# Kernel optimization log

Hardware: AMD Instinct MI355X
Metric: run time of the kernel (lower is better)

## Reference

```python
import jax, jax.numpy as jnp
import numpy as np

M = 16                      # multiplicity of each irrep block
INV3 = 1.0 / np.sqrt(3.0)   # w3j(1,1,0) component-normalized
INV2 = 1.0 / np.sqrt(2.0)   # w3j(1,1,1) component-normalized
A0 = 1.0 / np.sqrt(2.0 * M) # fan-in norm for 0e outputs (2 paths x mul 16)
A1 = 1.0 / np.sqrt(3.0 * M) # fan-in norm for 1o outputs (3 paths x mul 16)


def setup_inputs() -> dict:
    E, N, ED, HID = 100000, 10000, 32, 128
    WNUM = 2 * M * (2 * M) + 3 * M * M  # 1792 per-edge TP weights
    ks = jax.random.split(jax.random.key(0), 10)
    return {
        "dst": jax.random.randint(ks[0], (E,), 0, N),
        "x_src": jax.random.normal(ks[1], (E, 4 * M), jnp.float32),   # 16x0e+16x1o
        "x_dst": jax.random.normal(ks[2], (N, 4 * M), jnp.float32),
        "sh": jax.random.normal(ks[3], (E, 4), jnp.float32),          # 1x0e+1x1o
        "edge_attr": jax.random.normal(ks[4], (E, ED), jnp.float32),
        "We1": jax.random.normal(ks[5], (ED, HID), jnp.float32) / np.sqrt(ED),
        "be1": jnp.zeros((HID,), jnp.float32),
        "We2": jax.random.normal(ks[6], (HID, WNUM), jnp.float32) / np.sqrt(HID),
        "be2": jnp.zeros((WNUM,), jnp.float32),
        "Wr0": jax.random.normal(ks[7], (M, 2 * M), jnp.float32),     # 16x0e -> 32x0e
        "Wr1": jax.random.normal(ks[8], (M, M), jnp.float32),         # 16x1o -> 16x1o
    }


def _forward(dst, x_src, x_dst, sh, edge_attr, We1, be1, We2, be2, Wr0, Wr1):
    E = x_src.shape[0]
    N = x_dst.shape[0]
    o0 = 2 * M  # 32x0e tp output (scalars + gates)

    # edge MLP -> per-edge tensor-product weights [E, 1792]
    w = jax.nn.relu(edge_attr @ We1 + be1) @ We2 + be2
    i = 0
    w_ss = w[:, i:i + M * o0].reshape(E, M, o0); i += M * o0   # 0e x 0e -> 0e
    w_vv0 = w[:, i:i + M * o0].reshape(E, M, o0); i += M * o0  # 1o x 1o -> 0e
    w_sv = w[:, i:i + M * M].reshape(E, M, M); i += M * M      # 0e x 1o -> 1o
    w_vs = w[:, i:i + M * M].reshape(E, M, M); i += M * M      # 1o x 0e -> 1o
    w_vv1 = w[:, i:i + M * M].reshape(E, M, M)                 # 1o x 1o -> 1o

    s1 = x_src[:, :M]                       # [E, 16]
    v1 = x_src[:, M:].reshape(E, M, 3)      # [E, 16, 3]
    s2 = sh[:, 0]                           # [E]
    v2 = sh[:, 1:4]                         # [E, 3]

    # fully-connected tensor product with per-edge weights
    out0 = A0 * (jnp.einsum('em,emo->eo', s1 * s2[:, None], w_ss)
                 + INV3 * jnp.einsum('emc,ec,emo->eo', v1, v2, w_vv0))  # [E, 32]
    cross = jnp.cross(v1, v2[:, None, :])   # [E, 16, 3]
    out1 = A1 * (jnp.einsum('em,ec,emo->eoc', s1, v2, w_sv)
                 + jnp.einsum('emc,e,emo->eoc', v1, s2, w_vs)
                 + INV2 * jnp.einsum('emc,emo->eoc', cross, w_vv1))     # [E, 16, 3]
    msg = jnp.concatenate([out0, out1.reshape(E, -1)], axis=1)          # [E, 80]

    # scatter-mean over destination nodes
    ssum = jax.ops.segment_sum(msg, dst, num_segments=N)
    cnt = jax.ops.segment_sum(jnp.ones((E,), msg.dtype), dst, num_segments=N)
    msg = ssum / jnp.maximum(cnt, 1.0)[:, None]                          # [N, 80]

    # residual equivariant linear on x_dst
    sd = x_dst[:, :M]
    vd = x_dst[:, M:].reshape(N, M, 3)
    res0 = (sd @ Wr0) / np.sqrt(M)                                       # [N, 32]
    res1 = jnp.einsum('nmc,mo->noc', vd, Wr1) / np.sqrt(M)               # [N, 16, 3]
    msg = msg + jnp.concatenate([res0, res1.reshape(N, -1)], axis=1)

    # gate nonlinearity: relu(scalars), sigmoid(gates) * gated vectors
    scalars = jax.nn.relu(msg[:, :M])
    gates = jax.nn.sigmoid(msg[:, M:2 * M])
    gated = msg[:, 2 * M:].reshape(N, M, 3) * gates[:, :, None]
    return jnp.concatenate([scalars, gated.reshape(N, -1)], axis=1)      # [N, 64]


def reference(dst, x_src, x_dst, sh, edge_attr, We1, be1, We2, be2, Wr0, Wr1):
    return _forward(dst, x_src, x_dst, sh, edge_attr, We1, be1, We2, be2, Wr0, Wr1)
```

## Files before the change

### kernel.cpp

```cpp
#include <hip/hip_runtime.h>
#include <math.h>

#define WNUM 1792
#define HID 128

#define INV3C 0.5773502691896258f
#define INV2C 0.7071067811865476f
#define A0C   0.17677669529663687f
#define A1C   0.14433756729740643f
#define MAXDEG 64

typedef short bf8 __attribute__((ext_vector_type(8)));
typedef _Float16 f16x8 __attribute__((ext_vector_type(8)));
typedef _Float16 f16x4 __attribute__((ext_vector_type(4)));
typedef float f32x4 __attribute__((ext_vector_type(4)));

__device__ inline unsigned short f2bf(float f) {
  union { float f; unsigned u; } v; v.f = f;
  unsigned r = v.u + 0x7FFFu + ((v.u >> 16) & 1u);
  return (unsigned short)(r >> 16);
}
__device__ inline float bf2f(unsigned short h) {
  union { unsigned u; float f; } v; v.u = ((unsigned)h) << 16;
  return v.f;
}
__device__ inline float wscale(int t) {
  if (t < 32) return A0C;
  if (t < 64) return A0C * INV3C;
  if (t < 96) return A1C;
  return A1C * INV2C;
}

__global__ __launch_bounds__(256) void prep_kernel(
    const float* __restrict__ We1, const float* __restrict__ We2,
    const float* __restrict__ be2,
    unsigned short* __restrict__ we1x, _Float16* __restrict__ we2h,
    float* __restrict__ be2p, int* __restrict__ cntp, int N)
{
  int i = blockIdx.x * 256 + threadIdx.x;
  if (i < 28672) {
    int t = i >> 8, c = (i >> 6) & 3, lane = i & 63;
    int quad = lane >> 4, l15 = lane & 15;
    int col = t * 16 + l15;
    float sc = wscale(t);
    f16x8 v;
    #pragma unroll
    for (int j = 0; j < 8; ++j) {
      int k = c * 32 + quad * 8 + j;
      v[j] = (_Float16)(We2[(size_t)k * WNUM + col] * sc);
    }
    *(f16x8*)(we2h + (size_t)t * 2048 + c * 512 + lane * 8) = v;
  } else if (i < 29184) {
    int q = i - 28672;
    int c1 = q >> 6, lane = q & 63;
    int quad = lane >> 4, l15 = lane & 15;
    int col = c1 * 16 + l15;
    bf8 hh, ll;
    #pragma unroll
    for (int j = 0; j < 8; ++j) {
      int k = quad * 8 + j;
      float v = We1[k * HID + col];
      unsigned short hi = f2bf(v);
      hh[j] = (short)hi;
      ll[j] = (short)f2bf(v - bf2f(hi));
    }
    *(bf8*)(we1x + c1 * 1024 + lane * 8) = hh;
    *(bf8*)(we1x + c1 * 1024 + 512 + lane * 8) = ll;
  } else if (i < 30976) {
    int q = i - 29184;
    int t = q >> 4, l16 = q & 15;
    be2p[(t >> 1) * 32 + l16 * 2 + (t & 1)] = be2[q] * wscale(t);
  } else if (i < 30976 + N) {
    cntp[i - 30976] = 0;
  }
}

__device__ inline void chains2(const f16x8* a0, const f16x8* a1,
    f16x8 b0, f16x8 b1, f16x8 b2, f16x8 b3,
    f16x8 b4, f16x8 b5, f16x8 b6, f16x8 b7,
    float2 bias, f32x4* wa, f32x4* wb)
{
  f32x4 ca0 = {bias.x, bias.x, bias.x, bias.x};
  f32x4 cb0 = {bias.y, bias.y, bias.y, bias.y};
  f32x4 ca1 = ca0, cb1 = cb0;
  ca0 = __builtin_amdgcn_mfma_f32_16x16x32_f16(a0[0], b0, ca0, 0, 0, 0);
  cb0 = __builtin_amdgcn_mfma_f32_16x16x32_f16(a0[0], b4, cb0, 0, 0, 0);
  ca1 = __builtin_amdgcn_mfma_f32_16x16x32_f16(a1[0], b0, ca1, 0, 0, 0);
  cb1 = __builtin_amdgcn_mfma_f32_16x16x32_f16(a1[0], b4, cb1, 0, 0, 0);
  ca0 = __builtin_amdgcn_mfma_f32_16x16x32_f16(a0[1], b1, ca0, 0, 0, 0);
  cb0 = __builtin_amdgcn_mfma_f32_16x16x32_f16(a0[1], b5, cb0, 0, 0, 0);
  ca1 = __builtin_amdgcn_mfma_f32_16x16x32_f16(a1[1], b1, ca1, 0, 0, 0);
  cb1 = __builtin_amdgcn_mfma_f32_16x16x32_f16(a1[1], b5, cb1, 0, 0, 0);
  ca0 = __builtin_amdgcn_mfma_f32_16x16x32_f16(a0[2], b2, ca0, 0, 0, 0);
  cb0 = __builtin_amdgcn_mfma_f32_16x16x32_f16(a0[2], b6, cb0, 0, 0, 0);
  ca1 = __builtin_amdgcn_mfma_f32_16x16x32_f16(a1[2], b2, ca1, 0, 0, 0);
  cb1 = __builtin_amdgcn_mfma_f32_16x16x32_f16(a1[2], b6, cb1, 0, 0, 0);
  ca0 = __builtin_amdgcn_mfma_f32_16x16x32_f16(a0[3], b3, ca0, 0, 0, 0);
  cb0 = __builtin_amdgcn_mfma_f32_16x16x32_f16(a0[3], b7, cb0, 0, 0, 0);
  ca1 = __builtin_amdgcn_mfma_f32_16x16x32_f16(a1[3], b3, ca1, 0, 0, 0);
  cb1 = __builtin_amdgcn_mfma_f32_16x16x32_f16(a1[3], b7, cb1, 0, 0, 0);
  wa[0] = ca0; wb[0] = cb0; wa[1] = ca1; wb[1] = cb1;
}

#define LOADB_LDS(BASE) \
  f16x8 b0 = *(const f16x8*)((BASE)); \
  f16x8 b1 = *(const f16x8*)((BASE) + 512); \
  f16x8 b2 = *(const f16x8*)((BASE) + 1024); \
  f16x8 b3 = *(const f16x8*)((BASE) + 1536); \
  f16x8 b4 = *(const f16x8*)((BASE) + 2048); \
  f16x8 b5 = *(const f16x8*)((BASE) + 2560); \
  f16x8 b6 = *(const f16x8*)((BASE) + 3072); \
  f16x8 b7 = *(const f16x8*)((BASE) + 3584);

template <bool MSG>
__global__ __launch_bounds__(256, 2) void edge_kernel(
    const float* __restrict__ ea, const float* __restrict__ xsrc,
    const float* __restrict__ sh, const int* __restrict__ dst,
    const float* __restrict__ be1,
    const unsigned short* __restrict__ we1x, const _Float16* __restrict__ we2h,
    const float* __restrict__ be2p,
    float* __restrict__ outp,
    int* __restrict__ eidx, int* __restrict__ cntp, int E)
{
  const int lane = threadIdx.x & 63;
  const int w    = threadIdx.x >> 6;
  const int quad = lane >> 4;
  const int l16  = lane & 15;
  const int eb   = (blockIdx.x * 4 + w) * 32;

  __shared__ _Float16 Bsm[2][4096];
  __shared__ _Float16 h_s[4][32][136];
  __shared__ _Float16 fss_s[4][16][32];
  __shared__ _Float16 fvv_s[4][16][32];
  __shared__ _Float16 s1h_s[4][16][32];
  __shared__ _Float16 v1h_s[4][16][3][32];
  __shared__ float4 vq_s[4][32];

  #define STAGEB(ldsbuf, p) { \
    const _Float16* gsrc_ = we2h + (size_t)(p) * 4096; \
    __builtin_amdgcn_global_load_lds( \
      (const __attribute__((address_space(1))) void*)(gsrc_ + (w * 2) * 512 + lane * 8), \
      (__attribute__((address_space(3))) void*)((ldsbuf) + (w * 2) * 512), 16, 0, 0); \
    __builtin_amdgcn_global_load_lds( \
      (const __attribute__((address_space(1))) void*)(gsrc_ + (w * 2 + 1) * 512 + lane * 8), \
      (__attribute__((address_space(3))) void*)((ldsbuf) + (w * 2 + 1) * 512), 16, 0, 0); \
  }

  if (lane < 32) {
    int ge = eb + lane;
    if (ge < E) {
      int node = dst[ge];
      int pos = atomicAdd(cntp + node, 1);
      if (MSG) { if (pos < MAXDEG) eidx[node * MAXDEG + pos] = ge; }
    }
  }

  {
    int e2 = lane >> 1, mg = lane & 1;
    int ge = eb + e2;
    if (ge < E) {
      const float* xp = xsrc + (size_t)ge * 64;
      float4 sq0 = *(const float4*)(xp + mg * 8);
      float4 sq1 = *(const float4*)(xp + mg * 8 + 4);
      float s1a[8] = {sq0.x,sq0.y,sq0.z,sq0.w,sq1.x,sq1.y,sq1.z,sq1.w};
      const float* vp = xp + 16 + mg * 24;
      float la[24];
      #pragma unroll
      for (int qv = 0; qv < 6; ++qv) {
        float4 t = *(const float4*)(vp + qv * 4);
        la[qv*4+0] = t.x; la[qv*4+1] = t.y; la[qv*4+2] = t.z; la[qv*4+3] = t.w;
      }
      float4 shq = *(const float4*)(sh + (size_t)ge * 4);
      float s2 = shq.x, v2x = shq.y, v2y = shq.z, v2z = shq.w;
      #pragma unroll
      for (int mi = 0; mi < 8; ++mi) {
        int m = mg * 8 + mi;
        float v1x = la[mi*3], v1y = la[mi*3+1], v1z = la[mi*3+2];
        fss_s[w][m][e2] = (_Float16)(s1a[mi] * s2);
        fvv_s[w][m][e2] = (_Float16)(v1x*v2x + v1y*v2y + v1z*v2z);
        s1h_s[w][m][e2] = (_Float16)s1a[mi];
        v1h_s[w][m][0][e2] = (_Float16)v1x;
        v1h_s[w][m][1][e2] = (_Float16)v1y;
        v1h_s[w][m][2][e2] = (_Float16)v1z;
      }
      if (mg == 0) vq_s[w][e2] = make_float4(v2x, v2y, v2z, s2);
    } else {
      #pragma unroll
      for (int mi = 0; mi < 8; ++mi) {
        int m = mg * 8 + mi;
        fss_s[w][m][e2] = (_Float16)0.f;
        fvv_s[w][m][e2] = (_Float16)0.f;
        s1h_s[w][m][e2] = (_Float16)0.f;
        v1h_s[w][m][0][e2] = (_Float16)0.f;
        v1h_s[w][m][1][e2] = (_Float16)0.f;
        v1h_s[w][m][2][e2] = (_Float16)0.f;
      }
      if (mg == 0) vq_s[w][e2] = make_float4(0,0,0,0);
    }
  }

  {
    bf8 ah[2], al[2];
    #pragma unroll
    for (int g = 0; g < 2; ++g) {
      int gea = eb + g * 16 + l16; if (gea > E - 1) gea = E - 1;
      const float* ep = ea + (size_t)gea * 32 + quad * 8;
      float4 p0 = *(const float4*)ep;
      float4 p1 = *(const float4*)(ep + 4);
      float pv[8] = {p0.x,p0.y,p0.z,p0.w,p1.x,p1.y,p1.z,p1.w};
      #pragma unroll
      for (int j = 0; j < 8; ++j) {
        unsigned short hi = f2bf(pv[j]);
        ah[g][j] = (short)hi;
        al[g][j] = (short)f2bf(pv[j] - bf2f(hi));
      }
    }
    const unsigned short* wb1 = we1x + lane * 8;
    #pragma unroll 2
    for (int c = 0; c < 8; ++c) {
      bf8 bh = *(const bf8*)(wb1 + c * 1024);
      bf8 bl = *(const bf8*)(wb1 + c * 1024 + 512);
      float bias = be1[c * 16 + l16];
      #pragma unroll
      for (int g = 0; g < 2; ++g) {
        f32x4 hc = {bias, bias, bias, bias};
        hc = __builtin_amdgcn_mfma_f32_16x16x32_bf16(al[g], bh, hc, 0, 0, 0);
        hc = __builtin_amdgcn_mfma_f32_16x16x32_bf16(ah[g], bl, hc, 0, 0, 0);
        hc = __builtin_amdgcn_mfma_f32_16x16x32_bf16(ah[g], bh, hc, 0, 0, 0);
        #pragma unroll
        for (int r = 0; r < 4; ++r)
          h_s[w][g * 16 + quad * 4 + r][c * 16 + l16] = (_Float16)fmaxf(hc[r], 0.f);
      }
    }
  }

  STAGEB(&Bsm[0][0], 0)
  __syncthreads();

  f16x8 af[2][4];
  #pragma unroll
  for (int g = 0; g < 2; ++g)
    #pragma unroll
    for (int ch = 0; ch < 4; ++ch)
      af[g][ch] = *(const f16x8*)&h_s[w][g * 16 + l16][ch * 32 + quad * 8];

  const float* bp = be2p + l16 * 2;

  float m0a[2][4] = {{0,0,0,0},{0,0,0,0}}, m0b[2][4] = {{0,0,0,0},{0,0,0,0}};
  int p = 0;

  #pragma unroll 1
  for (int i = 0; i < 16; ++i) {
    STAGEB(&Bsm[(p + 1) & 1][0], p + 1)
    const _Float16* bL = &Bsm[p & 1][lane * 8];
    LOADB_LDS(bL)
    float2 bias2 = *(const float2*)(bp + p * 32);
    f32x4 wa[2], wb[2];
    chains2(af[0], af[1], b0,b1,b2,b3,b4,b5,b6,b7, bias2, wa, wb);
    #pragma unroll
    for (int g = 0; g < 2; ++g) {
      f16x4 fv = *(const f16x4*)&fss_s[w][i][g * 16 + quad * 4];
      #pragma unroll
      for (int r = 0; r < 4; ++r) {
        float f = (float)fv[r];
        m0a[g][r] = fmaf(wa[g][r], f, m0a[g][r]);
        m0b[g][r] = fmaf(wb[g][r], f, m0b[g][r]);
      }
    }
    __syncthreads();
    ++p;
  }

  #pragma unroll 1
  for (int i = 0; i < 16; ++i) {
    STAGEB(&Bsm[(p + 1) & 1][0], p + 1)
    const _Float16* bL = &Bsm[p & 1][lane * 8];
    LOADB_LDS(bL)
    float2 bias2 = *(const float2*)(bp + p * 32);
    f32x4 wa[2], wb[2];
    chains2(af[0], af[1], b0,b1,b2,b3,b4,b5,b6,b7, bias2, wa, wb);
    #pragma unroll
    for (int g = 0; g < 2; ++g) {
      f16x4 fv = *(const f16x4*)&fvv_s[w][i][g * 16 + quad * 4];
      #pragma unroll
      for (int r = 0; r < 4; ++r) {
        float f = (float)fv[r];
        m0a[g][r] = fmaf(wa[g][r], f, m0a[g][r]);
        m0b[g][r] = fmaf(wb[g][r], f, m0b[g][r]);
      }
    }
    __syncthreads();
    ++p;
  }

  #pragma unroll
  for (int g = 0; g < 2; ++g)
    #pragma unroll
    for (int r = 0; r < 4; ++r) {
      int ge = eb + g * 16 + quad * 4 + r;
      if (ge < E) {
        if (MSG) {
          float* mp = outp + (size_t)ge * 80;
          mp[l16]      = m0a[g][r];
          mp[16 + l16] = m0b[g][r];
        } else {
          float* ap = outp + (size_t)dst[ge] * 80;
          atomicAdd(ap + l16,      m0a[g][r]);
          atomicAdd(ap + 16 + l16, m0b[g][r]);
        }
      }
    }

  float sg[2][4] = {{0,0,0,0},{0,0,0,0}};
  #pragma unroll 1
  for (int i = 0; i < 8; ++i) {
    STAGEB(&Bsm[(p + 1) & 1][0], p + 1)
    const _Float16* bL = &Bsm[p & 1][lane * 8];
    LOADB_LDS(bL)
    float2 bias2 = *(const float2*)(bp + p * 32);
    f32x4 wa[2], wb[2];
    chains2(af[0], af[1], b0,b1,b2,b3,b4,b5,b6,b7, bias2, wa, wb);
    #pragma unroll
    for (int g = 0; g < 2; ++g) {
      f16x4 sA = *(const f16x4*)&s1h_s[w][2*i][g * 16 + quad * 4];
      f16x4 sB = *(const f16x4*)&s1h_s[w][2*i + 1][g * 16 + quad * 4];
      #pragma unroll
      for (int r = 0; r < 4; ++r)
        sg[g][r] = fmaf(wb[g][r], (float)sB[r], fmaf(wa[g][r], (float)sA[r], sg[g][r]));
    }
    __syncthreads();
    ++p;
  }
  float4 vq[2][4];
  #pragma unroll
  for (int g = 0; g < 2; ++g)
    #pragma unroll
    for (int r = 0; r < 4; ++r) vq[g][r] = vq_s[w][g * 16 + quad * 4 + r];

  float m1x[2][4], m1y[2][4], m1z[2][4];
  #pragma unroll
  for (int g = 0; g < 2; ++g)
    #pragma unroll
    for (int r = 0; r < 4; ++r) {
      m1x[g][r] = sg[g][r] * vq[g][r].x;
      m1y[g][r] = sg[g][r] * vq[g][r].y;
      m1z[g][r] = sg[g][r] * vq[g][r].z;
    }

  {
    float ux[2][4] = {{0,0,0,0},{0,0,0,0}}, uy[2][4] = {{0,0,0,0},{0,0,0,0}},
          uz[2][4] = {{0,0,0,0},{0,0,0,0}};
    #pragma unroll 1
    for (int i = 0; i < 8; ++i) {
      STAGEB(&Bsm[(p + 1) & 1][0], p + 1)
      const _Float16* bL = &Bsm[p & 1][lane * 8];
      LOADB_LDS(bL)
      float2 bias2 = *(const float2*)(bp + p * 32);
      f32x4 wa[2], wb[2];
      chains2(af[0], af[1], b0,b1,b2,b3,b4,b5,b6,b7, bias2, wa, wb);
      #pragma unroll
      for (int g = 0; g < 2; ++g) {
        f16x4 xA = *(const f16x4*)&v1h_s[w][2*i][0][g*16 + quad*4];
        f16x4 xB = *(const f16x4*)&v1h_s[w][2*i+1][0][g*16 + quad*4];
        f16x4 yA = *(const f16x4*)&v1h_s[w][2*i][1][g*16 + quad*4];
        f16x4 yB = *(const f16x4*)&v1h_s[w][2*i+1][1][g*16 + quad*4];
        f16x4 zA = *(const f16x4*)&v1h_s[w][2*i][2][g*16 + quad*4];
        f16x4 zB = *(const f16x4*)&v1h_s[w][2*i+1][2][g*16 + quad*4];
        #pragma unroll
        for (int r = 0; r < 4; ++r) {
          ux[g][r] = fmaf(wb[g][r], (float)xB[r], fmaf(wa[g][r], (float)xA[r], ux[g][r]));
          uy[g][r] = fmaf(wb[g][r], (float)yB[r], fmaf(wa[g][r], (float)yA[r], uy[g][r]));
          uz[g][r] = fmaf(wb[g][r], (float)zB[r], fmaf(wa[g][r], (float)zA[r], uz[g][r]));
        }
      }
      __syncthreads();
      ++p;
    }
    #pragma unroll
    for (int g = 0; g < 2; ++g)
      #pragma unroll
      for (int r = 0; r < 4; ++r) {
        m1x[g][r] = fmaf(vq[g][r].w, ux[g][r], m1x[g][r]);
        m1y[g][r] = fmaf(vq[g][r].w, uy[g][r], m1y[g][r]);
        m1z[g][r] = fmaf(vq[g][r].w, uz[g][r], m1z[g][r]);
      }
  }

  {
    float ux[2][4] = {{0,0,0,0},{0,0,0,0}}, uy[2][4] = {{0,0,0,0},{0,0,0,0}},
          uz[2][4] = {{0,0,0,0},{0,0,0,0}};
    #pragma unroll 1
    for (int i = 0; i < 8; ++i) {
      if (p + 1 < 56) STAGEB(&Bsm[(p + 1) & 1][0], p + 1)
      const _Float16* bL = &Bsm[p & 1][lane * 8];
      LOADB_LDS(bL)
      float2 bias2 = *(const float2*)(bp + p * 32);
      f32x4 wa[2], wb[2];
      chains2(af[0], af[1], b0,b1,b2,b3,b4,b5,b6,b7, bias2, wa, wb);
      #pragma unroll
      for (int g = 0; g < 2; ++g) {
        f16x4 xA = *(const f16x4*)&v1h_s[w][2*i][0][g*16 + quad*4];
        f16x4 xB = *(const f16x4*)&v1h_s[w][2*i+1][0][g*16 + quad*4];
        f16x4 yA = *(const f16x4*)&v1h_s[w][2*i][1][g*16 + quad*4];
        f16x4 yB = *(const f16x4*)&v1h_s[w][2*i+1][1][g*16 + quad*4];
        f16x4 zA = *(const f16x4*)&v1h_s[w][2*i][2][g*16 + quad*4];
        f16x4 zB = *(const f16x4*)&v1h_s[w][2*i+1][2][g*16 + quad*4];
        #pragma unroll
        for (int r = 0; r < 4; ++r) {
          ux[g][r] = fmaf(wb[g][r], (float)xB[r], fmaf(wa[g][r], (float)xA[r], ux[g][r]));
          uy[g][r] = fmaf(wb[g][r], (float)yB[r], fmaf(wa[g][r], (float)yA[r], uy[g][r]));
          uz[g][r] = fmaf(wb[g][r], (float)zB[r], fmaf(wa[g][r], (float)zA[r], uz[g][r]));
        }
      }
      __syncthreads();
      ++p;
    }
    #pragma unroll
    for (int g = 0; g < 2; ++g)
      #pragma unroll
      for (int r = 0; r < 4; ++r) {
        m1x[g][r] = fmaf(uy[g][r], vq[g][r].z, m1x[g][r]);
        m1x[g][r] = fmaf(-uz[g][r], vq[g][r].y, m1x[g][r]);
        m1y[g][r] = fmaf(uz[g][r], vq[g][r].x, m1y[g][r]);
        m1y[g][r] = fmaf(-ux[g][r], vq[g][r].z, m1y[g][r]);
        m1z[g][r] = fmaf(ux[g][r], vq[g][r].y, m1z[g][r]);
        m1z[g][r] = fmaf(-uy[g][r], vq[g][r].x, m1z[g][r]);
      }
  }

  #pragma unroll
  for (int g = 0; g < 2; ++g)
    #pragma unroll
    for (int r = 0; r < 4; ++r) {
      int ge = eb + g * 16 + quad * 4 + r;
      if (ge < E) {
        if (MSG) {
          float* mp = outp + (size_t)ge * 80;
          mp[32 + l16*3 + 0] = m1x[g][r];
          mp[32 + l16*3 + 1] = m1y[g][r];
          mp[32 + l16*3 + 2] = m1z[g][r];
        } else {
          float* ap = outp + (size_t)dst[ge] * 80;
          atomicAdd(ap + 32 + l16*3 + 0, m1x[g][r]);
          atomicAdd(ap + 32 + l16*3 + 1, m1y[g][r]);
          atomicAdd(ap + 32 + l16*3 + 2, m1z[g][r]);
        }
      }
    }
  #undef STAGEB
}

__global__ __launch_bounds__(128) void node_gather_kernel(
    const float* __restrict__ msg, const int* __restrict__ eidx,
    const int* __restrict__ cntp,
    const float* __restrict__ xdst, const float* __restrict__ Wr0,
    const float* __restrict__ Wr1, float* __restrict__ out, int N)
{
  int n = blockIdx.x;
  if (n >= N) return;
  int j = threadIdx.x;
  int c0 = cntp[n];
  int deg = c0 < MAXDEG ? c0 : MAXDEG;
  float inv = 1.0f / fmaxf((float)c0, 1.0f);
  __shared__ float s_sum[80];
  if (j < 80) {
    float s = 0.f;
    const int* ep = eidx + (size_t)n * MAXDEG;
    int i = 0;
    for (; i + 1 < deg; i += 2) {
      int e0 = ep[i], e1 = ep[i + 1];
      s += msg[(size_t)e0 * 80 + j] + msg[(size_t)e1 * 80 + j];
    }
    if (i < deg) s += msg[(size_t)ep[i] * 80 + j];
    s_sum[j] = s * inv;
  }
  __syncthreads();
  if (j >= 64) return;
  const float* xd = xdst + (size_t)n * 64;
  float* op = out + (size_t)n * 64;
  if (j < 16) {
    float s = 0.f;
    #pragma unroll
    for (int m = 0; m < 16; ++m) s = fmaf(xd[m], Wr0[m * 32 + j], s);
    op[j] = fmaxf(s_sum[j] + 0.25f * s, 0.f);
  } else {
    int jj = j - 16;
    int o = (jj * 86) >> 8;
    int c = jj - o * 3;
    float tg = 0.f, v = 0.f;
    #pragma unroll
    for (int m = 0; m < 16; ++m) {
      tg = fmaf(xd[m], Wr0[m * 32 + 16 + o], tg);
      v  = fmaf(xd[16 + m * 3 + c], Wr1[m * 16 + o], v);
    }
    float g = 1.0f / (1.0f + expf(-(s_sum[16 + o] + 0.25f * tg)));
    op[16 + jj] = (s_sum[32 + jj] + 0.25f * v) * g;
  }
}

__global__ __launch_bounds__(256) void node_kernel(
    const float* __restrict__ accn, const int* __restrict__ cntp,
    const float* __restrict__ xdst, const float* __restrict__ Wr0,
    const float* __restrict__ Wr1, float* __restrict__ out, int N)
{
  int idx = blockIdx.x * 256 + threadIdx.x;
  int n = idx >> 6, j = idx & 63;
  if (n >= N) return;
  float inv = 1.0f / fmaxf((float)cntp[n], 1.0f);
  const float* ap = accn + (size_t)n * 80;
  const float* xd = xdst + (size_t)n * 64;
  float* op = out + (size_t)n * 64;
  if (j < 16) {
    float s = 0.f;
    #pragma unroll
    for (int m = 0; m < 16; ++m) s = fmaf(xd[m], Wr0[m * 32 + j], s);
    op[j] = fmaxf(ap[j] * inv + 0.25f * s, 0.f);
  } else {
    int jj = j - 16;
    int o = (jj * 86) >> 8;
    int c = jj - o * 3;
    float tg = 0.f, v = 0.f;
    #pragma unroll
    for (int m = 0; m < 16; ++m) {
      tg = fmaf(xd[m], Wr0[m * 32 + 16 + o], tg);
      v  = fmaf(xd[16 + m * 3 + c], Wr1[m * 16 + o], v);
    }
    float g = 1.0f / (1.0f + expf(-(ap[16 + o] * inv + 0.25f * tg)));
    op[16 + jj] = (ap[32 + jj] * inv + 0.25f * v) * g;
  }
}

extern "C" void kernel_launch(void* const* d_in, const int* in_sizes, int n_in,
                              void* d_out, int out_size, void* d_ws, size_t ws_size,
                              hipStream_t stream)
{
  const int*   dst  = (const int*)d_in[0];
  const float* xsrc = (const float*)d_in[1];
  const float* xdst = (const float*)d_in[2];
  const float* sh   = (const float*)d_in[3];
  const float* ea   = (const float*)d_in[4];
  const float* We1  = (const float*)d_in[5];
  const float* be1  = (const float*)d_in[6];
  const float* We2  = (const float*)d_in[7];
  const float* be2  = (const float*)d_in[8];
  const float* Wr0  = (const float*)d_in[9];
  const float* Wr1  = (const float*)d_in[10];
  const int E = in_sizes[0];
  const int N = in_sizes[2] / 64;

  char* ws = (char*)d_ws;
  _Float16* we2h = (_Float16*)ws;
  unsigned short* we1x = (unsigned short*)(ws + 458752);
  float* be2p = (float*)(ws + 475136);
  int*   cntp = (int*)(ws + 482560);
  size_t off = 482560 + (size_t)N * 4;
  off = (off + 15) & ~(size_t)15;

  size_t need_msg = off + (size_t)N * MAXDEG * 4 + (size_t)E * 80 * 4;
  bool use_msg = (ws_size >= need_msg);

  prep_kernel<<<(30976 + N + 255) / 256, 256, 0, stream>>>(We1, We2, be2,
      we1x, we2h, be2p, cntp, N);

  if (use_msg) {
    int* eidx = (int*)(ws + off);
    float* msg = (float*)(ws + off + (size_t)N * MAXDEG * 4);
    edge_kernel<true><<<(E + 127) / 128, 256, 0, stream>>>(ea, xsrc, sh, dst, be1,
        we1x, we2h, be2p, msg, eidx, cntp, E);
    node_gather_kernel<<<N, 128, 0, stream>>>(msg, eidx, cntp, xdst, Wr0, Wr1,
        (float*)d_out, N);
  } else {
    float* accn = (float*)(ws + off);
    hipMemsetAsync(accn, 0, (size_t)N * 320, stream);
    edge_kernel<false><<<(E + 127) / 128, 256, 0, stream>>>(ea, xsrc, sh, dst, be1,
        we1x, we2h, be2p, accn, (int*)nullptr, cntp, E);
    node_kernel<<<((size_t)N * 64 + 255) / 256, 256, 0, stream>>>(accn, cntp,
        xdst, Wr0, Wr1, (float*)d_out, N);
  }
}
```

Measured before the change: 204.2 us.

## Stage We2 tiles in a 4-deep LDS ring and halve per-tile barriers

The double-buffered We2 staging buffer becomes a four-slot ring that shares LDS with the hidden-activation buffer through a union. Each loop iteration now processes two weight tiles and prefetches the next two, so a block barrier runs every two tiles instead of every tile. The goal is to cut synchronisation overhead and widen the prefetch distance without raising LDS use. The cost is an extra barrier before staging starts, to protect the reused h buffer, and a first load of two tiles that is exposed.

```diff
diff --git a/kernel.cpp b/kernel.cpp
--- a/kernel.cpp
+++ b/kernel.cpp
@@ -102,15 +102,20 @@
   wa[0] = ca0; wb[0] = cb0; wa[1] = ca1; wb[1] = cb1;
 }
 
-#define LOADB_LDS(BASE) \
-  f16x8 b0 = *(const f16x8*)((BASE)); \
-  f16x8 b1 = *(const f16x8*)((BASE) + 512); \
-  f16x8 b2 = *(const f16x8*)((BASE) + 1024); \
-  f16x8 b3 = *(const f16x8*)((BASE) + 1536); \
-  f16x8 b4 = *(const f16x8*)((BASE) + 2048); \
-  f16x8 b5 = *(const f16x8*)((BASE) + 2560); \
-  f16x8 b6 = *(const f16x8*)((BASE) + 3072); \
-  f16x8 b7 = *(const f16x8*)((BASE) + 3584);
+__device__ inline void pair_mm(const _Float16* bL, const float* bp, int p,
+                               const f16x8 (&af)[2][4], f32x4* wa, f32x4* wb)
+{
+  f16x8 b0 = *(const f16x8*)(bL);
+  f16x8 b1 = *(const f16x8*)(bL + 512);
+  f16x8 b2 = *(const f16x8*)(bL + 1024);
+  f16x8 b3 = *(const f16x8*)(bL + 1536);
+  f16x8 b4 = *(const f16x8*)(bL + 2048);
+  f16x8 b5 = *(const f16x8*)(bL + 2560);
+  f16x8 b6 = *(const f16x8*)(bL + 3072);
+  f16x8 b7 = *(const f16x8*)(bL + 3584);
+  float2 bias2 = *(const float2*)(bp + p * 32);
+  chains2(af[0], af[1], b0, b1, b2, b3, b4, b5, b6, b7, bias2, wa, wb);
+}
 
 template <bool MSG>
 __global__ __launch_bounds__(256, 2) void edge_kernel(
@@ -119,8 +124,7 @@
     const float* __restrict__ be1,
     const unsigned short* __restrict__ we1x, const _Float16* __restrict__ we2h,
     const float* __restrict__ be2p,
-    float* __restrict__ outp,
-    int* __restrict__ eidx, int* __restrict__ cntp, int E)
+    float* __restrict__ outp, int* __restrict__ eidx, int* __restrict__ cntp, int E)
 {
   const int lane = threadIdx.x & 63;
   const int w    = threadIdx.x >> 6;
@@ -128,22 +132,25 @@
   const int l16  = lane & 15;
   const int eb   = (blockIdx.x * 4 + w) * 32;
 
-  __shared__ _Float16 Bsm[2][4096];
-  __shared__ _Float16 h_s[4][32][136];
+  __shared__ union SMem {
+    _Float16 h[4][32][136];
+    _Float16 B[4][4096];
+  } uS;
   __shared__ _Float16 fss_s[4][16][32];
   __shared__ _Float16 fvv_s[4][16][32];
   __shared__ _Float16 s1h_s[4][16][32];
   __shared__ _Float16 v1h_s[4][16][3][32];
   __shared__ float4 vq_s[4][32];
 
-  #define STAGEB(ldsbuf, p) { \
+  #define STAGE_PAIR(p) { \
     const _Float16* gsrc_ = we2h + (size_t)(p) * 4096; \
+    _Float16* ldst_ = &uS.B[(p) & 3][0]; \
     __builtin_amdgcn_global_load_lds( \
       (const __attribute__((address_space(1))) void*)(gsrc_ + (w * 2) * 512 + lane * 8), \
-      (__attribute__((address_space(3))) void*)((ldsbuf) + (w * 2) * 512), 16, 0, 0); \
+      (__attribute__((address_space(3))) void*)(ldst_ + (w * 2) * 512), 16, 0, 0); \
     __builtin_amdgcn_global_load_lds( \
       (const __attribute__((address_space(1))) void*)(gsrc_ + (w * 2 + 1) * 512 + lane * 8), \
-      (__attribute__((address_space(3))) void*)((ldsbuf) + (w * 2 + 1) * 512), 16, 0, 0); \
+      (__attribute__((address_space(3))) void*)(ldst_ + (w * 2 + 1) * 512), 16, 0, 0); \
   }
 
   if (lane < 32) {
@@ -229,12 +236,10 @@
         hc = __builtin_amdgcn_mfma_f32_16x16x32_bf16(ah[g], bh, hc, 0, 0, 0);
         #pragma unroll
         for (int r = 0; r < 4; ++r)
-          h_s[w][g * 16 + quad * 4 + r][c * 16 + l16] = (_Float16)fmaxf(hc[r], 0.f);
-      }
-    }
-  }
-
-  STAGEB(&Bsm[0][0], 0)
+          uS.h[w][g * 16 + quad * 4 + r][c * 16 + l16] = (_Float16)fmaxf(hc[r], 0.f);
+      }
+    }
+  }
   __syncthreads();
 
   f16x8 af[2][4];
@@ -242,21 +247,22 @@
   for (int g = 0; g < 2; ++g)
     #pragma unroll
     for (int ch = 0; ch < 4; ++ch)
-      af[g][ch] = *(const f16x8*)&h_s[w][g * 16 + l16][ch * 32 + quad * 8];
+      af[g][ch] = *(const f16x8*)&uS.h[w][g * 16 + l16][ch * 32 + quad * 8];
+  __syncthreads();
+
+  STAGE_PAIR(0)
+  STAGE_PAIR(1)
+  __syncthreads();
 
   const float* bp = be2p + l16 * 2;
-
   float m0a[2][4] = {{0,0,0,0},{0,0,0,0}}, m0b[2][4] = {{0,0,0,0},{0,0,0,0}};
-  int p = 0;
 
   #pragma unroll 1
-  for (int i = 0; i < 16; ++i) {
-    STAGEB(&Bsm[(p + 1) & 1][0], p + 1)
-    const _Float16* bL = &Bsm[p & 1][lane * 8];
-    LOADB_LDS(bL)
-    float2 bias2 = *(const float2*)(bp + p * 32);
+  for (int i = 0; i < 16; i += 2) {
+    STAGE_PAIR(i + 2)
+    STAGE_PAIR(i + 3)
     f32x4 wa[2], wb[2];
-    chains2(af[0], af[1], b0,b1,b2,b3,b4,b5,b6,b7, bias2, wa, wb);
+    pair_mm(&uS.B[i & 3][lane * 8], bp, i, af, wa, wb);
     #pragma unroll
     for (int g = 0; g < 2; ++g) {
       f16x4 fv = *(const f16x4*)&fss_s[w][i][g * 16 + quad * 4];
@@ -267,21 +273,10 @@
         m0b[g][r] = fmaf(wb[g][r], f, m0b[g][r]);
       }
     }
-    __syncthreads();
-    ++p;
-  }
-
-  #pragma unroll 1
-  for (int i = 0; i < 16; ++i) {
-    STAGEB(&Bsm[(p + 1) & 1][0], p + 1)
-    const _Float16* bL = &Bsm[p & 1][lane * 8];
-    LOADB_LDS(bL)
-    float2 bias2 = *(const float2*)(bp + p * 32);
-    f32x4 wa[2], wb[2];
-    chains2(af[0], af[1], b0,b1,b2,b3,b4,b5,b6,b7, bias2, wa, wb);
+    pair_mm(&uS.B[(i + 1) & 3][lane * 8], bp, i + 1, af, wa, wb);
     #pragma unroll
     for (int g = 0; g < 2; ++g) {
-      f16x4 fv = *(const f16x4*)&fvv_s[w][i][g * 16 + quad * 4];
+      f16x4 fv = *(const f16x4*)&fss_s[w][i + 1][g * 16 + quad * 4];
       #pragma unroll
       for (int r = 0; r < 4; ++r) {
         float f = (float)fv[r];
@@ -290,7 +285,37 @@
       }
     }
     __syncthreads();
-    ++p;
+  }
+
+  #pragma unroll 1
+  for (int i = 0; i < 16; i += 2) {
+    int pg = 16 + i;
+    STAGE_PAIR(pg + 2)
+    STAGE_PAIR(pg + 3)
+    f32x4 wa[2], wb[2];
+    pair_mm(&uS.B[pg & 3][lane * 8], bp, pg, af, wa, wb);
+    #pragma unroll
+    for (int g = 0; g < 2; ++g) {
+      f16x4 fv = *(const f16x4*)&fvv_s[w][i][g * 16 + quad * 4];
+      #pragma unroll
+      for (int r = 0; r < 4; ++r) {
+        float f = (float)fv[r];
+        m0a[g][r] = fmaf(wa[g][r], f, m0a[g][r]);
+        m0b[g][r] = fmaf(wb[g][r], f, m0b[g][r]);
+      }
+    }
+    pair_mm(&uS.B[(pg + 1) & 3][lane * 8], bp, pg + 1, af, wa, wb);
+    #pragma unroll
+    for (int g = 0; g < 2; ++g) {
+      f16x4 fv = *(const f16x4*)&fvv_s[w][i + 1][g * 16 + quad * 4];
+      #pragma unroll
+      for (int r = 0; r < 4; ++r) {
+        float f = (float)fv[r];
+        m0a[g][r] = fmaf(wa[g][r], f, m0a[g][r]);
+        m0b[g][r] = fmaf(wb[g][r], f, m0b[g][r]);
+      }
+    }
+    __syncthreads();
   }
 
   #pragma unroll
@@ -313,13 +338,12 @@
 
   float sg[2][4] = {{0,0,0,0},{0,0,0,0}};
   #pragma unroll 1
-  for (int i = 0; i < 8; ++i) {
-    STAGEB(&Bsm[(p + 1) & 1][0], p + 1)
-    const _Float16* bL = &Bsm[p & 1][lane * 8];
-    LOADB_LDS(bL)
-    float2 bias2 = *(const float2*)(bp + p * 32);
+  for (int i = 0; i < 8; i += 2) {
+    int pg = 32 + i;
+    STAGE_PAIR(pg + 2)
+    STAGE_PAIR(pg + 3)
     f32x4 wa[2], wb[2];
-    chains2(af[0], af[1], b0,b1,b2,b3,b4,b5,b6,b7, bias2, wa, wb);
+    pair_mm(&uS.B[pg & 3][lane * 8], bp, pg, af, wa, wb);
     #pragma unroll
     for (int g = 0; g < 2; ++g) {
       f16x4 sA = *(const f16x4*)&s1h_s[w][2*i][g * 16 + quad * 4];
@@ -328,8 +352,16 @@
       for (int r = 0; r < 4; ++r)
         sg[g][r] = fmaf(wb[g][r], (float)sB[r], fmaf(wa[g][r], (float)sA[r], sg[g][r]));
     }
+    pair_mm(&uS.B[(pg + 1) & 3][lane * 8], bp, pg + 1, af, wa, wb);
+    #pragma unroll
+    for (int g = 0; g < 2; ++g) {
+      f16x4 sA = *(const f16x4*)&s1h_s[w][2*i + 2][g * 16 + quad * 4];
+      f16x4 sB = *(const f16x4*)&s1h_s[w][2*i + 3][g * 16 + quad * 4];
+      #pragma unroll
+      for (int r = 0; r < 4; ++r)
+        sg[g][r] = fmaf(wb[g][r], (float)sB[r], fmaf(wa[g][r], (float)sA[r], sg[g][r]));
+    }
     __syncthreads();
-    ++p;
   }
   float4 vq[2][4];
   #pragma unroll
@@ -347,17 +379,18 @@
       m1z[g][r] = sg[g][r] * vq[g][r].z;
     }
 
-  {
+  #pragma unroll
+  for (int sec = 0; sec < 2; ++sec) {
     float ux[2][4] = {{0,0,0,0},{0,0,0,0}}, uy[2][4] = {{0,0,0,0},{0,0,0,0}},
           uz[2][4] = {{0,0,0,0},{0,0,0,0}};
+    int base = 40 + sec * 8;
     #pragma unroll 1
-    for (int i = 0; i < 8; ++i) {
-      STAGEB(&Bsm[(p + 1) & 1][0], p + 1)
-      const _Float16* bL = &Bsm[p & 1][lane * 8];
-      LOADB_LDS(bL)
-      float2 bias2 = *(const float2*)(bp + p * 32);
+    for (int i = 0; i < 8; i += 2) {
+      int pg = base + i;
+      if (pg + 2 < 56) STAGE_PAIR(pg + 2)
+      if (pg + 3 < 56) STAGE_PAIR(pg + 3)
       f32x4 wa[2], wb[2];
-      chains2(af[0], af[1], b0,b1,b2,b3,b4,b5,b6,b7, bias2, wa, wb);
+      pair_mm(&uS.B[pg & 3][lane * 8], bp, pg, af, wa, wb);
       #pragma unroll
       for (int g = 0; g < 2; ++g) {
         f16x4 xA = *(const f16x4*)&v1h_s[w][2*i][0][g*16 + quad*4];
@@ -373,38 +406,15 @@
           uz[g][r] = fmaf(wb[g][r], (float)zB[r], fmaf(wa[g][r], (float)zA[r], uz[g][r]));
         }
       }
-      __syncthreads();
-      ++p;
-    }
-    #pragma unroll
-    for (int g = 0; g < 2; ++g)
-      #pragma unroll
-      for (int r = 0; r < 4; ++r) {
-        m1x[g][r] = fmaf(vq[g][r].w, ux[g][r], m1x[g][r]);
-        m1y[g][r] = fmaf(vq[g][r].w, uy[g][r], m1y[g][r]);
-        m1z[g][r] = fmaf(vq[g][r].w, uz[g][r], m1z[g][r]);
-      }
-  }
-
-  {
-    float ux[2][4] = {{0,0,0,0},{0,0,0,0}}, uy[2][4] = {{0,0,0,0},{0,0,0,0}},
-          uz[2][4] = {{0,0,0,0},{0,0,0,0}};
-    #pragma unroll 1
-    for (int i = 0; i < 8; ++i) {
-      if (p + 1 < 56) STAGEB(&Bsm[(p + 1) & 1][0], p + 1)
-      const _Float16* bL = &Bsm[p & 1][lane * 8];
-      LOADB_LDS(bL)
-      float2 bias2 = *(const float2*)(bp + p * 32);
-      f32x4 wa[2], wb[2];
-      chains2(af[0], af[1], b0,b1,b2,b3,b4,b5,b6,b7, bias2, wa, wb);
+      pair_mm(&uS.B[(pg + 1) & 3][lane * 8], bp, pg + 1, af, wa, wb);
       #pragma unroll
       for (int g = 0; g < 2; ++g) {
-        f16x4 xA = *(const f16x4*)&v1h_s[w][2*i][0][g*16 + quad*4];
-        f16x4 xB = *(const f16x4*)&v1h_s[w][2*i+1][0][g*16 + quad*4];
-        f16x4 yA = *(const f16x4*)&v1h_s[w][2*i][1][g*16 + quad*4];
-        f16x4 yB = *(const f16x4*)&v1h_s[w][2*i+1][1][g*16 + quad*4];
-        f16x4 zA = *(const f16x4*)&v1h_s[w][2*i][2][g*16 + quad*4];
-        f16x4 zB = *(const f16x4*)&v1h_s[w][2*i+1][2][g*16 + quad*4];
+        f16x4 xA = *(const f16x4*)&v1h_s[w][2*i+2][0][g*16 + quad*4];
+        f16x4 xB = *(const f16x4*)&v1h_s[w][2*i+3][0][g*16 + quad*4];
+        f16x4 yA = *(const f16x4*)&v1h_s[w][2*i+2][1][g*16 + quad*4];
+        f16x4 yB = *(const f16x4*)&v1h_s[w][2*i+3][1][g*16 + quad*4];
+        f16x4 zA = *(const f16x4*)&v1h_s[w][2*i+2][2][g*16 + quad*4];
+        f16x4 zB = *(const f16x4*)&v1h_s[w][2*i+3][2][g*16 + quad*4];
         #pragma unroll
         for (int r = 0; r < 4; ++r) {
           ux[g][r] = fmaf(wb[g][r], (float)xB[r], fmaf(wa[g][r], (float)xA[r], ux[g][r]));
@@ -413,19 +423,29 @@
         }
       }
       __syncthreads();
-      ++p;
-    }
-    #pragma unroll
-    for (int g = 0; g < 2; ++g)
-      #pragma unroll
-      for (int r = 0; r < 4; ++r) {
-        m1x[g][r] = fmaf(uy[g][r], vq[g][r].z, m1x[g][r]);
-        m1x[g][r] = fmaf(-uz[g][r], vq[g][r].y, m1x[g][r]);
-        m1y[g][r] = fmaf(uz[g][r], vq[g][r].x, m1y[g][r]);
-        m1y[g][r] = fmaf(-ux[g][r], vq[g][r].z, m1y[g][r]);
-        m1z[g][r] = fmaf(ux[g][r], vq[g][r].y, m1z[g][r]);
-        m1z[g][r] = fmaf(-uy[g][r], vq[g][r].x, m1z[g][r]);
-      }
+    }
+    if (sec == 0) {
+      #pragma unroll
+      for (int g = 0; g < 2; ++g)
+        #pragma unroll
+        for (int r = 0; r < 4; ++r) {
+          m1x[g][r] = fmaf(vq[g][r].w, ux[g][r], m1x[g][r]);
+          m1y[g][r] = fmaf(vq[g][r].w, uy[g][r], m1y[g][r]);
+          m1z[g][r] = fmaf(vq[g][r].w, uz[g][r], m1z[g][r]);
+        }
+    } else {
+      #pragma unroll
+      for (int g = 0; g < 2; ++g)
+        #pragma unroll
+        for (int r = 0; r < 4; ++r) {
+          m1x[g][r] = fmaf(uy[g][r], vq[g][r].z, m1x[g][r]);
+          m1x[g][r] = fmaf(-uz[g][r], vq[g][r].y, m1x[g][r]);
+          m1y[g][r] = fmaf(uz[g][r], vq[g][r].x, m1y[g][r]);
+          m1y[g][r] = fmaf(-ux[g][r], vq[g][r].z, m1y[g][r]);
+          m1z[g][r] = fmaf(ux[g][r], vq[g][r].y, m1z[g][r]);
+          m1z[g][r] = fmaf(-uy[g][r], vq[g][r].x, m1z[g][r]);
+        }
+    }
   }
 
   #pragma unroll
@@ -447,7 +467,7 @@
         }
       }
     }
-  #undef STAGEB
+  #undef STAGE_PAIR
 }
 
 __global__ __launch_bounds__(128) void node_gather_kernel(
```

Result: faster. 199.5 us (-2.3%).
